# Kernel tuning notes

Hardware: AMD Instinct MI355X
Metric: run time of the kernel (lower is better)

Reference implementation:

```python
import jax, jax.numpy as jnp
import numpy as np

GRAPH_BIAS_SCALE = 0.8
COMMITMENT_COST = 0.01

B, S, L, N = 4, 2048, 512, 8192
D = 2 * L  # codebook feature dim


def setup_inputs() -> dict:
    key = jax.random.key(0)
    ks = jax.random.split(key, 9)
    gw_real = jax.random.normal(ks[0], (B, S, L), dtype=jnp.float32)
    gw_imag = jax.random.normal(ks[1], (B, S, L), dtype=jnp.float32)
    prev_symbol_idx = jax.random.randint(ks[2], (B, S), 0, N)
    codebook = jax.random.uniform(ks[3], (N, D), jnp.float32, -0.5, 0.5)
    adjacency = 0.1 * jax.random.normal(ks[4], (N, N), dtype=jnp.float32)
    sal_w = 0.02 * jax.random.normal(ks[5], (D, 1), dtype=jnp.float32)
    sal_b = jnp.zeros((1,), jnp.float32)
    conf_w = 0.02 * jax.random.normal(ks[6], (D, 1), dtype=jnp.float32)
    conf_b = jnp.zeros((1,), jnp.float32)
    return dict(gw_real=gw_real, gw_imag=gw_imag, prev_symbol_idx=prev_symbol_idx,
                codebook=codebook, adjacency=adjacency,
                sal_w=sal_w, sal_b=sal_b, conf_w=conf_w, conf_b=conf_b)


def reference(gw_real, gw_imag, prev_symbol_idx, codebook, adjacency,
              sal_w, sal_b, conf_w, conf_b):
    sg = jax.lax.stop_gradient
    # z_flat = cat(real, imag): [B, S, D]
    z = jnp.concatenate([gw_real, gw_imag], axis=-1)
    # squared euclidean distances to codebook: [B, S, N]
    d = (jnp.sum(z * z, axis=-1, keepdims=True)
         + jnp.sum(codebook * codebook, axis=-1)
         - 2.0 * jnp.einsum('bsd,nd->bsn', z, codebook))
    # graph prior bias from adjacency rows of previous symbols
    graph_prior = adjacency[prev_symbol_idx]            # [B, S, N]
    d = d - GRAPH_BIAS_SCALE * jax.nn.sigmoid(graph_prior)
    min_indices = jnp.argmin(d, axis=-1)                # [B, S]
    z_q = codebook[min_indices]                         # [B, S, D]
    loss_vq = jnp.mean((z_q - sg(z)) ** 2)
    loss_commit = jnp.mean((sg(z_q) - z) ** 2)
    # straight-through estimator
    z_q_st = z + sg(z_q - z)
    dist_score = -jnp.min(d, axis=-1, keepdims=True)    # [B, S, 1]
    salience = z_q_st @ sal_w + sal_b + 0.1 * dist_score
    confidence = jax.nn.sigmoid(z_q_st @ conf_w + conf_b)
    total_loss = loss_vq + COMMITMENT_COST * loss_commit
    proposal_real = z_q_st[..., :L]
    proposal_imag = z_q_st[..., L:]
    return (proposal_real, proposal_imag, salience, confidence, total_loss, min_indices)
```

## Files before the change

### kernel.cpp

```cpp
#include <hip/hip_runtime.h>
#include <math.h>

#define RDIM 8192
#define DDIM 1024
#define NDIM 8192
#define LDIM 512
#define KT 16

#define OFF_REAL 0
#define OFF_IMAG 4194304
#define OFF_SAL  8388608
#define OFF_CONF 8396800
#define OFF_LOSS 8404992
#define OFF_IDX  8404993

#define MAXCAND 64
#define MARGIN_Q 76
#define QSCALE 64.0f
#define FLT_BIG 3.4e38f

typedef __attribute__((ext_vector_type(8))) short bf16x8;
typedef __attribute__((ext_vector_type(8))) short short8v;
typedef __attribute__((ext_vector_type(4))) float f32x4;

__device__ __forceinline__ unsigned short f2bf(float x) {
  unsigned u = __builtin_bit_cast(unsigned, x);
  unsigned r = (u + 0x7fff + ((u >> 16) & 1)) >> 16;
  return (unsigned short)r;
}

__device__ __forceinline__ void load_lds16(const void* g, void* l) {
  __builtin_amdgcn_global_load_lds((const __attribute__((address_space(1))) void*)g,
                                   (__attribute__((address_space(3))) void*)l, 16, 0, 0);
}

__device__ __forceinline__ short clampq(float s) {
  int qi = __float2int_rn(s * QSCALE);
  qi = qi > 32767 ? 32767 : (qi < -32767 ? -32767 : qi);
  return (short)qi;
}

__global__ __launch_bounds__(256)
void split_norms_kernel(const float* __restrict__ gw_real, const float* __restrict__ gw_imag,
                        const float* __restrict__ codebook,
                        unsigned short* __restrict__ zh, unsigned short* __restrict__ ch,
                        float* __restrict__ znorm, float* __restrict__ cnorm) {
  const int w = threadIdx.x >> 6, l = threadIdx.x & 63;
  const int id = blockIdx.x * 4 + w;
  const float* src;
  unsigned short* dst;
  float* nrm;
  int row;
  if (id < RDIM) {
    row = id; dst = zh; nrm = znorm;
    src = (l < 32) ? gw_real + (size_t)row * LDIM + l * 16
                   : gw_imag + (size_t)row * LDIM + (l - 32) * 16;
  } else {
    row = id - RDIM; dst = ch; nrm = cnorm;
    src = codebook + (size_t)row * DDIM + l * 16;
  }
  float f[16];
#pragma unroll
  for (int i = 0; i < 4; ++i) {
    const float4 v = reinterpret_cast<const float4*>(src)[i];
    f[i*4+0] = v.x; f[i*4+1] = v.y; f[i*4+2] = v.z; f[i*4+3] = v.w;
  }
  short8v h0, h1;
  float s = 0.f;
#pragma unroll
  for (int i = 0; i < 8; ++i) { h0[i] = (short)f2bf(f[i]);     s += f[i] * f[i]; }
#pragma unroll
  for (int i = 0; i < 8; ++i) { h1[i] = (short)f2bf(f[8 + i]); s += f[8+i] * f[8+i]; }
  unsigned short* dp = dst + (size_t)row * DDIM + l * 16;
  *reinterpret_cast<short8v*>(dp)     = h0;
  *reinterpret_cast<short8v*>(dp + 8) = h1;
#pragma unroll
  for (int m = 1; m < 64; m <<= 1) s += __shfl_xor(s, m, 64);
  if (l == 0) nrm[row] = s;
}

#define STAGE(basep, kt, ldsbyte) do {                                        \
    load_lds16((basep) + eo1 + (kt) * 64, L + (ldsbyte) + wid * 1024);        \
    load_lds16((basep) + eo2 + (kt) * 64, L + (ldsbyte) + 8192 + wid * 1024); \
  } while (0)

__global__ __launch_bounds__(512)
void dist_mfma_kernel(const unsigned short* __restrict__ zh, const unsigned short* __restrict__ ch,
                      const float* __restrict__ cnorm, short* __restrict__ q) {
  __shared__ unsigned short ldsbuf[65536];
  char* const L = (char*)ldsbuf;

  const int sidx = (int)blockIdx.x;
  const int sw = (sidx & 7) * 128 + (sidx >> 3);
  const int bm = sw >> 5, bn = sw & 31;
  const int row0 = bm * 256, col0 = bn * 256;

  const int tid = threadIdx.x;
  const int wid = tid >> 6, l = tid & 63;
  const int wm = wid >> 2, wn = wid & 3;
  const int lr = l & 15, lg = l >> 4;

  const int p1 = tid, p2 = tid + 512;
  const int r1 = p1 >> 3, c1 = (p1 & 7) ^ (r1 & 7);
  const int r2 = p2 >> 3, c2 = (p2 & 7) ^ (r2 & 7);
  const int eo1 = r1 * DDIM + c1 * 8;
  const int eo2 = r2 * DDIM + c2 * 8;
  const unsigned short* const az0 = zh + (size_t)row0 * DDIM;
  const unsigned short* const az1 = zh + (size_t)(row0 + 128) * DDIM;
  const unsigned short* const ac0 = ch + (size_t)col0 * DDIM;
  const unsigned short* const ac1 = ch + (size_t)(col0 + 128) * DDIM;

  const int fo0 = lr * 128 + ((lg ^ (lr & 7)) << 4);
  const int fo1 = fo0 ^ 64;

  f32x4 acc[4][8];
#pragma unroll
  for (int i = 0; i < 4; ++i)
#pragma unroll
    for (int j = 0; j < 8; ++j)
      acc[i][j] = (f32x4){0.f, 0.f, 0.f, 0.f};

  bf16x8 cfA[2][2], cfB[2][2], zf[4][2];

  STAGE(az0, 0, 0);
  STAGE(az1, 0, 16384);
  STAGE(ac0, 0, 32768);
  STAGE(ac1, 0, 49152);
  STAGE(ac0, 1, 98304);
  STAGE(ac1, 1, 114688);
  asm volatile("s_waitcnt vmcnt(4)" ::: "memory");
  __builtin_amdgcn_sched_barrier(0);
  __builtin_amdgcn_s_barrier();

  for (int t = 0; t < KT; ++t) {
    const int buf = t & 1, nbuf = buf ^ 1;
    const char* const Ab = L + buf * 65536 + wm * 16384;
    const char* const Bb = L + buf * 65536 + 32768 + wn * 8192;

#pragma unroll
    for (int i = 0; i < 2; ++i) {
      cfA[i][0] = *reinterpret_cast<const bf16x8*>(Bb + i * 2048 + fo0);
      cfA[i][1] = *reinterpret_cast<const bf16x8*>(Bb + i * 2048 + fo1);
    }
#pragma unroll
    for (int j = 0; j < 4; ++j) {
      zf[j][0] = *reinterpret_cast<const bf16x8*>(Ab + j * 2048 + fo0);
      zf[j][1] = *reinterpret_cast<const bf16x8*>(Ab + j * 2048 + fo1);
    }
    if (t + 1 < KT) STAGE(az0, t + 1, nbuf * 65536);
    __builtin_amdgcn_sched_barrier(0);
    __builtin_amdgcn_s_barrier();
    __builtin_amdgcn_s_setprio(1);
#pragma unroll
    for (int kh = 0; kh < 2; ++kh)
#pragma unroll
      for (int i = 0; i < 2; ++i)
#pragma unroll
        for (int j = 0; j < 4; ++j)
          acc[i][j] = __builtin_amdgcn_mfma_f32_16x16x32_bf16(cfA[i][kh], zf[j][kh], acc[i][j], 0, 0, 0);
    __builtin_amdgcn_s_setprio(0);
    __builtin_amdgcn_sched_barrier(0);
    __builtin_amdgcn_s_barrier();

#pragma unroll
    for (int i = 0; i < 2; ++i) {
      cfB[i][0] = *reinterpret_cast<const bf16x8*>(Bb + (2 + i) * 2048 + fo0);
      cfB[i][1] = *reinterpret_cast<const bf16x8*>(Bb + (2 + i) * 2048 + fo1);
    }
    if (t + 1 < KT) STAGE(az1, t + 1, nbuf * 65536 + 16384);
    __builtin_amdgcn_sched_barrier(0);
    __builtin_amdgcn_s_barrier();
    __builtin_amdgcn_s_setprio(1);
#pragma unroll
    for (int kh = 0; kh < 2; ++kh)
#pragma unroll
      for (int i = 0; i < 2; ++i)
#pragma unroll
        for (int j = 0; j < 4; ++j)
          acc[2 + i][j] = __builtin_amdgcn_mfma_f32_16x16x32_bf16(cfB[i][kh], zf[j][kh], acc[2 + i][j], 0, 0, 0);
    __builtin_amdgcn_s_setprio(0);
    __builtin_amdgcn_sched_barrier(0);
    __builtin_amdgcn_s_barrier();

#pragma unroll
    for (int j = 0; j < 4; ++j) {
      zf[j][0] = *reinterpret_cast<const bf16x8*>(Ab + (4 + j) * 2048 + fo0);
      zf[j][1] = *reinterpret_cast<const bf16x8*>(Ab + (4 + j) * 2048 + fo1);
    }
    if (t + 2 < KT) STAGE(ac0, t + 2, buf * 65536 + 32768);
    __builtin_amdgcn_sched_barrier(0);
    __builtin_amdgcn_s_barrier();
    __builtin_amdgcn_s_setprio(1);
#pragma unroll
    for (int kh = 0; kh < 2; ++kh)
#pragma unroll
      for (int i = 0; i < 2; ++i)
#pragma unroll
        for (int j = 0; j < 4; ++j)
          acc[2 + i][4 + j] = __builtin_amdgcn_mfma_f32_16x16x32_bf16(cfB[i][kh], zf[j][kh], acc[2 + i][4 + j], 0, 0, 0);
    __builtin_amdgcn_s_setprio(0);
    __builtin_amdgcn_sched_barrier(0);
    __builtin_amdgcn_s_barrier();

    if (t + 2 < KT) STAGE(ac1, t + 2, buf * 65536 + 49152);
    if (t < KT - 2) { asm volatile("s_waitcnt vmcnt(4)" ::: "memory"); }
    else            { asm volatile("s_waitcnt vmcnt(0)" ::: "memory"); }
    __builtin_amdgcn_sched_barrier(0);
    __builtin_amdgcn_s_barrier();
    __builtin_amdgcn_s_setprio(1);
#pragma unroll
    for (int kh = 0; kh < 2; ++kh)
#pragma unroll
      for (int i = 0; i < 2; ++i)
#pragma unroll
        for (int j = 0; j < 4; ++j)
          acc[i][4 + j] = __builtin_amdgcn_mfma_f32_16x16x32_bf16(cfA[i][kh], zf[j][kh], acc[i][4 + j], 0, 0, 0);
    __builtin_amdgcn_s_setprio(0);
    __builtin_amdgcn_sched_barrier(0);
    __builtin_amdgcn_s_barrier();
  }

  const int czero = col0 + wn * 64;
  const int zzero = row0 + wm * 128;
#pragma unroll
  for (int i = 0; i < 4; ++i) {
    const int cc = czero + i * 16 + lg * 4;
    const float4 cn4 = *reinterpret_cast<const float4*>(cnorm + cc);
#pragma unroll
    for (int j = 0; j < 8; ++j) {
      const int zr = zzero + j * 16 + lr;
      const f32x4 a = acc[i][j];
      *reinterpret_cast<short4*>(q + (size_t)zr * NDIM + cc) =
          make_short4(clampq(cn4.x - 2.0f * a[0]), clampq(cn4.y - 2.0f * a[1]),
                      clampq(cn4.z - 2.0f * a[2]), clampq(cn4.w - 2.0f * a[3]));
    }
  }
}

__global__ __launch_bounds__(256)
void collect_refine_kernel(const short* __restrict__ q, const int* __restrict__ prev,
                           const float* __restrict__ adj,
                           const float* __restrict__ gw_real, const float* __restrict__ gw_imag,
                           const float* __restrict__ codebook,
                           const float* __restrict__ znorm, const float* __restrict__ cnorm,
                           float* __restrict__ out, float* __restrict__ minfinal,
                           int* __restrict__ idxfinal) {
  __shared__ unsigned s_wmin[4];
  __shared__ int s_cnt;
  __shared__ int s_list[MAXCAND];
  __shared__ float s_bv[4];
  __shared__ int   s_bi[4];
  const int row = blockIdx.x;
  const int t = threadIdx.x;
  if (t == 0) s_cnt = 0;
  short8v v[4];
  unsigned kmin = 0xffffffffu;
#pragma unroll
  for (int c = 0; c < 4; ++c) {
    v[c] = *reinterpret_cast<const short8v*>(q + (size_t)row * NDIM + (c * 256 + t) * 8);
#pragma unroll
    for (int j = 0; j < 8; ++j) {
      const int col = (c * 256 + t) * 8 + j;
      const unsigned key = (((unsigned)((int)v[c][j] + 32768)) << 13) | (unsigned)col;
      kmin = (key < kmin) ? key : kmin;
    }
  }
  for (int m = 1; m < 64; m <<= 1) {
    const unsigned o = (unsigned)__shfl_xor((int)kmin, m, 64);
    kmin = (o < kmin) ? o : kmin;
  }
  if ((t & 63) == 0) s_wmin[t >> 6] = kmin;
  __syncthreads();
  unsigned gk = s_wmin[0];
  gk = gk < s_wmin[1] ? gk : s_wmin[1];
  gk = gk < s_wmin[2] ? gk : s_wmin[2];
  gk = gk < s_wmin[3] ? gk : s_wmin[3];
  const int qmin = (int)(gk >> 13) - 32768;
  const int winner = (int)(gk & 8191u);
  const int thr = qmin + MARGIN_Q;
#pragma unroll
  for (int c = 0; c < 4; ++c) {
#pragma unroll
    for (int j = 0; j < 8; ++j) {
      if ((int)v[c][j] <= thr) {
        const int pos = atomicAdd(&s_cnt, 1);
        if (pos < MAXCAND) s_list[pos] = (c * 256 + t) * 8 + j;
      }
    }
  }
  __syncthreads();
  const int cnt = (s_cnt < MAXCAND) ? s_cnt : MAXCAND;
  if (cnt <= 1) {
    if (t == 0) {
      const int p = prev[row];
      const float bias = 0.8f / (1.0f + expf(-adj[(size_t)p * NDIM + winner]));
      out[OFF_IDX + row] = (float)winner;
      idxfinal[row] = winner;
      minfinal[row] = znorm[row] + (float)qmin * (1.0f / QSCALE) - bias;
    }
    return;
  }
  const int w = t >> 6, l = t & 63;
  const int base = l * 16;
  const float* zp = (base < LDIM) ? gw_real + (size_t)row * LDIM + base
                                  : gw_imag + (size_t)row * LDIM + (base - LDIM);
  float z[16];
#pragma unroll
  for (int c = 0; c < 4; ++c) {
    const float4 zv = reinterpret_cast<const float4*>(zp)[c];
    z[c*4+0] = zv.x; z[c*4+1] = zv.y; z[c*4+2] = zv.z; z[c*4+3] = zv.w;
  }
  const float zn = znorm[row];
  const int p = prev[row];
  float bestd = FLT_BIG;
  int besti = 0x7fffffff;
  for (int j = w; j < cnt; j += 4) {
    const int idx = s_list[j];
    const float* cp = codebook + (size_t)idx * DDIM + base;
    float dot = 0.f;
#pragma unroll
    for (int c = 0; c < 4; ++c) {
      const float4 cv = reinterpret_cast<const float4*>(cp)[c];
      dot += z[c*4+0]*cv.x + z[c*4+1]*cv.y + z[c*4+2]*cv.z + z[c*4+3]*cv.w;
    }
    for (int m = 1; m < 64; m <<= 1) dot += __shfl_xor(dot, m, 64);
    const float d = zn + cnorm[idx] - 2.0f * dot
                  - 0.8f / (1.0f + expf(-adj[(size_t)p * NDIM + idx]));
    if (d < bestd || (d == bestd && idx < besti)) { bestd = d; besti = idx; }
  }
  if (l == 0) { s_bv[w] = bestd; s_bi[w] = besti; }
  __syncthreads();
  if (t == 0) {
    float bv = s_bv[0]; int bi = s_bi[0];
#pragma unroll
    for (int w2 = 1; w2 < 4; ++w2) {
      const float ov = s_bv[w2]; const int oi = s_bi[w2];
      if (ov < bv || (ov == bv && oi < bi)) { bv = ov; bi = oi; }
    }
    out[OFF_IDX + row] = (float)bi;
    minfinal[row] = bv;
    idxfinal[row] = bi;
  }
}


__global__ __launch_bounds__(256)
void epilogue_kernel(const float* __restrict__ gw_real, const float* __restrict__ gw_imag,
                     const float* __restrict__ codebook,
                     const float* __restrict__ sal_w, const float* __restrict__ sal_b,
                     const float* __restrict__ conf_w, const float* __restrict__ conf_b,
                     const float* __restrict__ minfinal, const int* __restrict__ idxfinal,
                     float* __restrict__ out, float* __restrict__ rowloss) {
  __shared__ float s1[4], s2[4], s3[4];
  const int row = blockIdx.x;
  const int t = threadIdx.x;
  const int w = t >> 6, l = t & 63;
  const int k = t << 2;
  const int idx = idxfinal[row];
  const float4 qv = *reinterpret_cast<const float4*>(codebook + (size_t)idx * DDIM + k);
  float4 z;
  if (k < LDIM) z = *reinterpret_cast<const float4*>(gw_real + (size_t)row * LDIM + k);
  else          z = *reinterpret_cast<const float4*>(gw_imag + (size_t)row * LDIM + (k - LDIM));
  const float dx = qv.x - z.x, dy = qv.y - z.y, dz = qv.z - z.z, dw = qv.w - z.w;
  float4 st;
  st.x = z.x + dx; st.y = z.y + dy; st.z = z.z + dz; st.w = z.w + dw;
  float* dst = (k < LDIM) ? (out + OFF_REAL + (size_t)row * LDIM + k)
                          : (out + OFF_IMAG + (size_t)row * LDIM + (k - LDIM));
  *reinterpret_cast<float4*>(dst) = st;
  const float4 sw = *reinterpret_cast<const float4*>(sal_w + k);
  const float4 cw = *reinterpret_cast<const float4*>(conf_w + k);
  float r1 = st.x*sw.x + st.y*sw.y + st.z*sw.z + st.w*sw.w;
  float r2 = st.x*cw.x + st.y*cw.y + st.z*cw.z + st.w*cw.w;
  float r3 = dx*dx + dy*dy + dz*dz + dw*dw;
#pragma unroll
  for (int m = 1; m < 64; m <<= 1) {
    r1 += __shfl_xor(r1, m, 64);
    r2 += __shfl_xor(r2, m, 64);
    r3 += __shfl_xor(r3, m, 64);
  }
  if (l == 0) { s1[w] = r1; s2[w] = r2; s3[w] = r3; }
  __syncthreads();
  if (t == 0) {
    const float t1 = s1[0] + s1[1] + s1[2] + s1[3];
    const float t2 = s2[0] + s2[1] + s2[2] + s2[3];
    const float t3 = s3[0] + s3[1] + s3[2] + s3[3];
    out[OFF_SAL + row]  = t1 + sal_b[0] + 0.1f * (-minfinal[row]);
    out[OFF_CONF + row] = 1.0f / (1.0f + expf(-(t2 + conf_b[0])));
    rowloss[row] = t3;
  }
}

__global__ __launch_bounds__(256)
void loss_kernel(const float* __restrict__ rowloss, float* __restrict__ out) {
  const int t = threadIdx.x;
  float s = 0.f;
  for (int i = t; i < RDIM; i += 256) s += rowloss[i];
  __shared__ float red[256];
  red[t] = s;
  __syncthreads();
  for (int st = 128; st > 0; st >>= 1) {
    if (t < st) red[t] += red[t + st];
    __syncthreads();
  }
  if (t == 0) {
    const float m = red[0] / (float)((size_t)RDIM * DDIM);
    out[OFF_LOSS] = m + 0.01f * m;
  }
}


__global__ __launch_bounds__(256)
void norms_kernel(const float* __restrict__ gw_real, const float* __restrict__ gw_imag,
                  const float* __restrict__ codebook,
                  float* __restrict__ znorm, float* __restrict__ cnorm) {
  const int id = blockIdx.x;
  const int t = threadIdx.x;
  float s;
  if (id < RDIM) {
    const float4* zr = reinterpret_cast<const float4*>(gw_real + (size_t)id * LDIM);
    const float4* zi = reinterpret_cast<const float4*>(gw_imag + (size_t)id * LDIM);
    const float4 v = (t < 128) ? zr[t] : zi[t - 128];
    s = v.x*v.x + v.y*v.y + v.z*v.z + v.w*v.w;
  } else {
    const float4* c = reinterpret_cast<const float4*>(codebook + (size_t)(id - RDIM) * DDIM);
    const float4 v = c[t];
    s = v.x*v.x + v.y*v.y + v.z*v.z + v.w*v.w;
  }
  __shared__ float red[256];
  red[t] = s;
  __syncthreads();
  for (int st = 128; st > 0; st >>= 1) {
    if (t < st) red[t] += red[t + st];
    __syncthreads();
  }
  if (t == 0) {
    if (id < RDIM) znorm[id] = red[0];
    else           cnorm[id - RDIM] = red[0];
  }
}

__global__ __launch_bounds__(256)
void dist_kernel(const float* __restrict__ gw_real, const float* __restrict__ gw_imag,
                 const float* __restrict__ codebook, const int* __restrict__ prev,
                 const float* __restrict__ adj, const float* __restrict__ znorm,
                 const float* __restrict__ cnorm,
                 float* __restrict__ ws_min, int* __restrict__ ws_idx) {
  __shared__ float As[16][64];
  __shared__ float Bs[16][64];
  __shared__ int prevs[64];
  const int bm = blockIdx.x, bn = blockIdx.y;
  const int row0 = bm * 64, col0 = bn * 64;
  const int tid = threadIdx.x;
  const int tx = tid & 15, ty = tid >> 4;
  if (tid < 64) prevs[tid] = prev[row0 + tid];
  const int lm = tid >> 2;
  const int lk = (tid & 3) << 2;
  const int arow = row0 + lm;
  const int brow = col0 + lm;
  float acc[4][4] = {{0.f,0.f,0.f,0.f},{0.f,0.f,0.f,0.f},{0.f,0.f,0.f,0.f},{0.f,0.f,0.f,0.f}};
  for (int kk = 0; kk < DDIM; kk += 16) {
    const int k = kk + lk;
    float4 a, b;
    if (k < LDIM) a = *reinterpret_cast<const float4*>(gw_real + (size_t)arow * LDIM + k);
    else          a = *reinterpret_cast<const float4*>(gw_imag + (size_t)arow * LDIM + (k - LDIM));
    b = *reinterpret_cast<const float4*>(codebook + (size_t)brow * DDIM + k);
    __syncthreads();
    As[lk+0][lm]=a.x; As[lk+1][lm]=a.y; As[lk+2][lm]=a.z; As[lk+3][lm]=a.w;
    Bs[lk+0][lm]=b.x; Bs[lk+1][lm]=b.y; Bs[lk+2][lm]=b.z; Bs[lk+3][lm]=b.w;
    __syncthreads();
#pragma unroll
    for (int k2 = 0; k2 < 16; ++k2) {
      const float4 a4 = *reinterpret_cast<const float4*>(&As[k2][ty << 2]);
      const float4 b4 = *reinterpret_cast<const float4*>(&Bs[k2][tx << 2]);
      const float av[4] = {a4.x, a4.y, a4.z, a4.w};
      const float bv[4] = {b4.x, b4.y, b4.z, b4.w};
#pragma unroll
      for (int i = 0; i < 4; ++i)
#pragma unroll
        for (int j = 0; j < 4; ++j)
          acc[i][j] = fmaf(av[i], bv[j], acc[i][j]);
    }
  }
  const float4 cn4 = *reinterpret_cast<const float4*>(cnorm + col0 + (tx << 2));
  const float cnv[4] = {cn4.x, cn4.y, cn4.z, cn4.w};
#pragma unroll
  for (int i = 0; i < 4; ++i) {
    const int rsub = (ty << 2) + i;
    const int row = row0 + rsub;
    const float zn = znorm[row];
    const int p = prevs[rsub];
    const float4 ad4 = *reinterpret_cast<const float4*>(adj + (size_t)p * NDIM + col0 + (tx << 2));
    const float adv[4] = {ad4.x, ad4.y, ad4.z, ad4.w};
    float bv = FLT_BIG;
    int bi = -1;
#pragma unroll
    for (int j = 0; j < 4; ++j) {
      const float bias = 0.8f * (1.0f / (1.0f + expf(-adv[j])));
      const float dv = (zn + cnv[j]) - 2.0f * acc[i][j] - bias;
      const int col = col0 + (tx << 2) + j;
      if (dv < bv) { bv = dv; bi = col; }
    }
    for (int m = 1; m < 16; m <<= 1) {
      const float ov = __shfl_xor(bv, m, 64);
      const int   oi = __shfl_xor(bi, m, 64);
      if (ov < bv || (ov == bv && oi < bi)) { bv = ov; bi = oi; }
    }
    if (tx == 0) {
      ws_min[(size_t)row * 128 + bn] = bv;
      ws_idx[(size_t)row * 128 + bn] = bi;
    }
  }
}

__global__ __launch_bounds__(128)
void argmin_reduce(const float* __restrict__ ws_min, const int* __restrict__ ws_idx,
                   float* __restrict__ out, float* __restrict__ minfinal,
                   int* __restrict__ idxfinal) {
  const int row = blockIdx.x;
  const int t = threadIdx.x;
  __shared__ float sv[128];
  __shared__ int   si[128];
  sv[t] = ws_min[(size_t)row * 128 + t];
  si[t] = ws_idx[(size_t)row * 128 + t];
  __syncthreads();
  for (int s = 64; s > 0; s >>= 1) {
    if (t < s) {
      const float ov = sv[t + s];
      const int   oi = si[t + s];
      if (ov < sv[t] || (ov == sv[t] && oi < si[t])) { sv[t] = ov; si[t] = oi; }
    }
    __syncthreads();
  }
  if (t == 0) {
    out[OFF_IDX + row] = (float)si[0];
    minfinal[row] = sv[0];
    idxfinal[row] = si[0];
  }
}


extern "C" void kernel_launch(void* const* d_in, const int* in_sizes, int n_in,
                              void* d_out, int out_size, void* d_ws, size_t ws_size,
                              hipStream_t stream) {
  const float* gw_real  = (const float*)d_in[0];
  const float* gw_imag  = (const float*)d_in[1];
  const int*   prev     = (const int*)d_in[2];
  const float* codebook = (const float*)d_in[3];
  const float* adj      = (const float*)d_in[4];
  const float* sal_w    = (const float*)d_in[5];
  const float* sal_b    = (const float*)d_in[6];
  const float* conf_w   = (const float*)d_in[7];
  const float* conf_b   = (const float*)d_in[8];
  float* out = (float*)d_out;
  char* ws = (char*)d_ws;

  const size_t matsz = (size_t)RDIM * DDIM;
  const size_t qsz   = (size_t)RDIM * NDIM;
  size_t need = 2 * matsz * 2
              + qsz * 2
              + 5 * (size_t)RDIM * 4 + 4096;

  if (ws_size >= need) {
    unsigned short* zh = (unsigned short*)ws;
    unsigned short* chh = zh + matsz;
    short* q = (short*)(chh + matsz);
    float* znorm    = (float*)(q + qsz);
    float* cnorm    = znorm + RDIM;
    float* minfinal = cnorm + NDIM;
    int*   idxfinal = (int*)(minfinal + RDIM);
    float* rowloss  = (float*)(idxfinal + RDIM);

    split_norms_kernel<<<(RDIM + NDIM) / 4, 256, 0, stream>>>(gw_real, gw_imag, codebook,
                                                              zh, chh, znorm, cnorm);
    dist_mfma_kernel<<<1024, 512, 0, stream>>>(zh, chh, cnorm, q);
    collect_refine_kernel<<<RDIM, 256, 0, stream>>>(q, prev, adj, gw_real, gw_imag, codebook,
                                                    znorm, cnorm, out, minfinal, idxfinal);
    epilogue_kernel<<<RDIM, 256, 0, stream>>>(gw_real, gw_imag, codebook, sal_w, sal_b,
                                              conf_w, conf_b, minfinal, idxfinal, out, rowloss);
    loss_kernel<<<1, 256, 0, stream>>>(rowloss, out);
  } else {
    float* ws_min   = (float*)ws;
    int*   ws_idx   = (int*)(ws + (size_t)RDIM * 128 * 4);
    float* znorm    = (float*)(ws + (size_t)RDIM * 128 * 8);
    float* cnorm    = znorm + RDIM;
    float* minfinal = cnorm + NDIM;
    int*   idxfinal = (int*)(minfinal + RDIM);
    float* rowloss  = (float*)(idxfinal + RDIM);

    norms_kernel<<<RDIM + NDIM, 256, 0, stream>>>(gw_real, gw_imag, codebook, znorm, cnorm);
    dist_kernel<<<dim3(RDIM / 64, NDIM / 64), 256, 0, stream>>>(
        gw_real, gw_imag, codebook, prev, adj, znorm, cnorm, ws_min, ws_idx);
    argmin_reduce<<<RDIM, 128, 0, stream>>>(ws_min, ws_idx, out, minfinal, idxfinal);
    epilogue_kernel<<<RDIM, 256, 0, stream>>>(gw_real, gw_imag, codebook, sal_w, sal_b,
                                              conf_w, conf_b, minfinal, idxfinal, out, rowloss);
    loss_kernel<<<1, 256, 0, stream>>>(rowloss, out);
  }
}
```

Before: 223.5 us.

## Fuse per-slice min and candidate masks into GEMM epilogue, drop quantized distance matrix

The GEMM epilogue no longer writes the full 8192x8192 int16 quantized distance matrix (128 MB). Each wave instead reduces its 64-column slice to a packed min key and a 64-bit mask of columns within the margin of that local min. The collect kernel then reads 128 keys and selected masks per row, using one wave instead of four, and refines the candidates serially. This removes most of the global memory traffic between the two kernels, at the cost of more shuffle work in the GEMM epilogue and less parallelism in refinement.

Result: faster. 195.3 us (-12.6%).

```diff
diff --git a/kernel.cpp b/kernel.cpp
--- a/kernel.cpp
+++ b/kernel.cpp
@@ -34,10 +34,10 @@
                                    (__attribute__((address_space(3))) void*)l, 16, 0, 0);
 }
 
-__device__ __forceinline__ short clampq(float s) {
+__device__ __forceinline__ int qbias(float s) {
   int qi = __float2int_rn(s * QSCALE);
   qi = qi > 32767 ? 32767 : (qi < -32767 ? -32767 : qi);
-  return (short)qi;
+  return qi + 32768;
 }
 
 __global__ __launch_bounds__(256)
@@ -86,7 +86,8 @@
 
 __global__ __launch_bounds__(512)
 void dist_mfma_kernel(const unsigned short* __restrict__ zh, const unsigned short* __restrict__ ch,
-                      const float* __restrict__ cnorm, short* __restrict__ q) {
+                      const float* __restrict__ cnorm,
+                      unsigned* __restrict__ keys, unsigned long long* __restrict__ masks) {
   __shared__ unsigned short ldsbuf[65536];
   char* const L = (char*)ldsbuf;
 
@@ -222,69 +223,94 @@
 
   const int czero = col0 + wn * 64;
   const int zzero = row0 + wm * 128;
+  const int slice = bn * 4 + wn;
+  float cnv[4][4];
 #pragma unroll
   for (int i = 0; i < 4; ++i) {
-    const int cc = czero + i * 16 + lg * 4;
-    const float4 cn4 = *reinterpret_cast<const float4*>(cnorm + cc);
-#pragma unroll
-    for (int j = 0; j < 8; ++j) {
-      const int zr = zzero + j * 16 + lr;
-      const f32x4 a = acc[i][j];
-      *reinterpret_cast<short4*>(q + (size_t)zr * NDIM + cc) =
-          make_short4(clampq(cn4.x - 2.0f * a[0]), clampq(cn4.y - 2.0f * a[1]),
-                      clampq(cn4.z - 2.0f * a[2]), clampq(cn4.w - 2.0f * a[3]));
-    }
-  }
-}
-
-__global__ __launch_bounds__(256)
-void collect_refine_kernel(const short* __restrict__ q, const int* __restrict__ prev,
-                           const float* __restrict__ adj,
+    const float4 c4 = *reinterpret_cast<const float4*>(cnorm + czero + i * 16 + lg * 4);
+    cnv[i][0] = c4.x; cnv[i][1] = c4.y; cnv[i][2] = c4.z; cnv[i][3] = c4.w;
+  }
+#pragma unroll
+  for (int j = 0; j < 8; ++j) {
+    const int row = zzero + j * 16 + lr;
+    int qv[16];
+    unsigned kmin = 0xffffffffu;
+#pragma unroll
+    for (int i = 0; i < 4; ++i)
+#pragma unroll
+      for (int reg = 0; reg < 4; ++reg) {
+        const int col = czero + i * 16 + lg * 4 + reg;
+        const int qb = qbias(cnv[i][reg] - 2.0f * acc[i][j][reg]);
+        qv[i * 4 + reg] = qb;
+        const unsigned key = ((unsigned)qb << 13) | (unsigned)col;
+        kmin = key < kmin ? key : kmin;
+      }
+    {
+      unsigned o = (unsigned)__shfl_xor((int)kmin, 16, 64);
+      kmin = o < kmin ? o : kmin;
+      o = (unsigned)__shfl_xor((int)kmin, 32, 64);
+      kmin = o < kmin ? o : kmin;
+    }
+    const int thr = (int)(kmin >> 13) + MARGIN_Q;
+    unsigned mlo = 0, mhi = 0;
+#pragma unroll
+    for (int i = 0; i < 4; ++i) {
+      unsigned nib = 0;
+#pragma unroll
+      for (int reg = 0; reg < 4; ++reg)
+        if (qv[i * 4 + reg] <= thr) nib |= 1u << reg;
+      const int sh = i * 16 + lg * 4;
+      if (i < 2) mlo |= nib << sh;
+      else       mhi |= nib << (sh - 32);
+    }
+    mlo |= (unsigned)__shfl_xor((int)mlo, 16, 64);
+    mlo |= (unsigned)__shfl_xor((int)mlo, 32, 64);
+    mhi |= (unsigned)__shfl_xor((int)mhi, 16, 64);
+    mhi |= (unsigned)__shfl_xor((int)mhi, 32, 64);
+    if (lg == 0) {
+      keys[(size_t)slice * RDIM + row] = kmin;
+      masks[(size_t)slice * RDIM + row] = ((unsigned long long)mhi << 32) | (unsigned long long)mlo;
+    }
+  }
+}
+
+__global__ __launch_bounds__(64)
+void collect_refine_kernel(const unsigned* __restrict__ keys,
+                           const unsigned long long* __restrict__ masks,
+                           const int* __restrict__ prev, const float* __restrict__ adj,
                            const float* __restrict__ gw_real, const float* __restrict__ gw_imag,
                            const float* __restrict__ codebook,
                            const float* __restrict__ znorm, const float* __restrict__ cnorm,
                            float* __restrict__ out, float* __restrict__ minfinal,
                            int* __restrict__ idxfinal) {
-  __shared__ unsigned s_wmin[4];
+  __shared__ int s_list[MAXCAND];
   __shared__ int s_cnt;
-  __shared__ int s_list[MAXCAND];
-  __shared__ float s_bv[4];
-  __shared__ int   s_bi[4];
   const int row = blockIdx.x;
   const int t = threadIdx.x;
   if (t == 0) s_cnt = 0;
-  short8v v[4];
-  unsigned kmin = 0xffffffffu;
-#pragma unroll
-  for (int c = 0; c < 4; ++c) {
-    v[c] = *reinterpret_cast<const short8v*>(q + (size_t)row * NDIM + (c * 256 + t) * 8);
-#pragma unroll
-    for (int j = 0; j < 8; ++j) {
-      const int col = (c * 256 + t) * 8 + j;
-      const unsigned key = (((unsigned)((int)v[c][j] + 32768)) << 13) | (unsigned)col;
-      kmin = (key < kmin) ? key : kmin;
-    }
-  }
+  __syncthreads();
+  const unsigned k0 = keys[(size_t)(2 * t) * RDIM + row];
+  const unsigned k1 = keys[(size_t)(2 * t + 1) * RDIM + row];
+  unsigned kmin = k0 < k1 ? k0 : k1;
+#pragma unroll
   for (int m = 1; m < 64; m <<= 1) {
     const unsigned o = (unsigned)__shfl_xor((int)kmin, m, 64);
-    kmin = (o < kmin) ? o : kmin;
-  }
-  if ((t & 63) == 0) s_wmin[t >> 6] = kmin;
-  __syncthreads();
-  unsigned gk = s_wmin[0];
-  gk = gk < s_wmin[1] ? gk : s_wmin[1];
-  gk = gk < s_wmin[2] ? gk : s_wmin[2];
-  gk = gk < s_wmin[3] ? gk : s_wmin[3];
-  const int qmin = (int)(gk >> 13) - 32768;
-  const int winner = (int)(gk & 8191u);
-  const int thr = qmin + MARGIN_Q;
-#pragma unroll
-  for (int c = 0; c < 4; ++c) {
-#pragma unroll
-    for (int j = 0; j < 8; ++j) {
-      if ((int)v[c][j] <= thr) {
+    kmin = o < kmin ? o : kmin;
+  }
+  const int qmin_b = (int)(kmin >> 13);
+  const int winner = (int)(kmin & 8191u);
+  const int thr = qmin_b + MARGIN_Q;
+#pragma unroll
+  for (int s2 = 0; s2 < 2; ++s2) {
+    const int s = 2 * t + s2;
+    const unsigned key = s2 ? k1 : k0;
+    if ((int)(key >> 13) <= thr) {
+      unsigned long long m = masks[(size_t)s * RDIM + row];
+      while (m) {
+        const int b = __builtin_ctzll(m);
+        m &= m - 1;
         const int pos = atomicAdd(&s_cnt, 1);
-        if (pos < MAXCAND) s_list[pos] = (c * 256 + t) * 8 + j;
+        if (pos < MAXCAND) s_list[pos] = s * 64 + b;
       }
     }
   }
@@ -296,12 +322,11 @@
       const float bias = 0.8f / (1.0f + expf(-adj[(size_t)p * NDIM + winner]));
       out[OFF_IDX + row] = (float)winner;
       idxfinal[row] = winner;
-      minfinal[row] = znorm[row] + (float)qmin * (1.0f / QSCALE) - bias;
+      minfinal[row] = znorm[row] + (float)(qmin_b - 32768) * (1.0f / QSCALE) - bias;
     }
     return;
   }
-  const int w = t >> 6, l = t & 63;
-  const int base = l * 16;
+  const int base = t * 16;
   const float* zp = (base < LDIM) ? gw_real + (size_t)row * LDIM + base
                                   : gw_imag + (size_t)row * LDIM + (base - LDIM);
   float z[16];
@@ -314,7 +339,7 @@
   const int p = prev[row];
   float bestd = FLT_BIG;
   int besti = 0x7fffffff;
-  for (int j = w; j < cnt; j += 4) {
+  for (int j = 0; j < cnt; ++j) {
     const int idx = s_list[j];
     const float* cp = codebook + (size_t)idx * DDIM + base;
     float dot = 0.f;
@@ -328,18 +353,10 @@
                   - 0.8f / (1.0f + expf(-adj[(size_t)p * NDIM + idx]));
     if (d < bestd || (d == bestd && idx < besti)) { bestd = d; besti = idx; }
   }
-  if (l == 0) { s_bv[w] = bestd; s_bi[w] = besti; }
-  __syncthreads();
   if (t == 0) {
-    float bv = s_bv[0]; int bi = s_bi[0];
-#pragma unroll
-    for (int w2 = 1; w2 < 4; ++w2) {
-      const float ov = s_bv[w2]; const int oi = s_bi[w2];
-      if (ov < bv || (ov == bv && oi < bi)) { bv = ov; bi = oi; }
-    }
-    out[OFF_IDX + row] = (float)bi;
-    minfinal[row] = bv;
-    idxfinal[row] = bi;
+    out[OFF_IDX + row] = (float)besti;
+    minfinal[row] = bestd;
+    idxfinal[row] = besti;
   }
 }
 
@@ -554,17 +571,18 @@
   float* out = (float*)d_out;
   char* ws = (char*)d_ws;
 
-  const size_t matsz = (size_t)RDIM * DDIM;
-  const size_t qsz   = (size_t)RDIM * NDIM;
+  const size_t matsz  = (size_t)RDIM * DDIM;
+  const size_t nslice = (size_t)RDIM * 128;
   size_t need = 2 * matsz * 2
-              + qsz * 2
+              + nslice * 4 + nslice * 8
               + 5 * (size_t)RDIM * 4 + 4096;
 
   if (ws_size >= need) {
     unsigned short* zh = (unsigned short*)ws;
     unsigned short* chh = zh + matsz;
-    short* q = (short*)(chh + matsz);
-    float* znorm    = (float*)(q + qsz);
+    unsigned* keys = (unsigned*)(chh + matsz);
+    unsigned long long* masks = (unsigned long long*)(keys + nslice);
+    float* znorm    = (float*)(masks + nslice);
     float* cnorm    = znorm + RDIM;
     float* minfinal = cnorm + NDIM;
     int*   idxfinal = (int*)(minfinal + RDIM);
@@ -572,9 +590,10 @@
 
     split_norms_kernel<<<(RDIM + NDIM) / 4, 256, 0, stream>>>(gw_real, gw_imag, codebook,
                                                               zh, chh, znorm, cnorm);
-    dist_mfma_kernel<<<1024, 512, 0, stream>>>(zh, chh, cnorm, q);
-    collect_refine_kernel<<<RDIM, 256, 0, stream>>>(q, prev, adj, gw_real, gw_imag, codebook,
-                                                    znorm, cnorm, out, minfinal, idxfinal);
+    dist_mfma_kernel<<<1024, 512, 0, stream>>>(zh, chh, cnorm, keys, masks);
+    collect_refine_kernel<<<RDIM, 64, 0, stream>>>(keys, masks, prev, adj,
+                                                   gw_real, gw_imag, codebook,
+                                                   znorm, cnorm, out, minfinal, idxfinal);
     epilogue_kernel<<<RDIM, 256, 0, stream>>>(gw_real, gw_imag, codebook, sal_w, sal_b,
                                               conf_w, conf_b, minfinal, idxfinal, out, rowloss);
     loss_kernel<<<1, 256, 0, stream>>>(rowloss, out);
```
